# Performance work log

Measured on AMD Instinct MI355X. Metric: run time of the kernel, lower is better.

## Reference

```python
import jax, jax.numpy as jnp
import numpy as np

B, S, D = 4, 2048, 768
LN_EPS = 1e-12


def setup_inputs() -> dict:
    key = jax.random.key(0)
    k0, k1, k2, k3 = jax.random.split(key, 4)
    scale = 1.0 / np.sqrt(D).astype(np.float32)
    return {
        "hidden_states": jax.random.normal(k0, (B, S, D), jnp.float32),
        "attention_mask": jnp.ones((B, 1, S, S), jnp.int32),
        "prior_n_attn": jax.random.uniform(k1, (B, S, S), jnp.float32),
        "ln_w": jnp.ones((D,), jnp.float32),
        "ln_b": jnp.zeros((D,), jnp.float32),
        "wq": jax.random.normal(k2, (D, D), jnp.float32) * scale,
        "bq": jnp.zeros((D,), jnp.float32),
        "wk": jax.random.normal(k3, (D, D), jnp.float32) * scale,
        "bk": jnp.zeros((D,), jnp.float32),
    }


def reference(hidden_states, attention_mask, prior_n_attn, ln_w, ln_b, wq, bq, wk, bk):
    _, S_, D_ = hidden_states.shape
    # LayerNorm (biased variance, as torch.nn.LayerNorm)
    mu = hidden_states.mean(-1, keepdims=True)
    var = ((hidden_states - mu) ** 2).mean(-1, keepdims=True)
    h = (hidden_states - mu) / jnp.sqrt(var + LN_EPS) * ln_w + ln_b

    a = jnp.eye(S_, k=1, dtype=jnp.int32)      # superdiagonal
    bI = jnp.eye(S_, dtype=jnp.int32)          # diagonal
    c = jnp.eye(S_, k=-1, dtype=jnp.int32)     # subdiagonal
    tri = jnp.triu(jnp.ones((S_, S_), jnp.float32))

    # mask & (a + c): band of width 1 off the diagonal; then squeeze dim 1
    mask = (attention_mask.astype(jnp.int32) & (a + c))[:, 0]  # [B,S,S]

    q = h @ wq + bq
    k = h @ wk + bk
    scores = jnp.einsum("bsd,btd->bst", q, k) / D_
    scores = jnp.where(mask == 0, -jnp.inf, scores)
    n = jnp.nan_to_num(jax.nn.softmax(scores, axis=-1))
    n = jnp.sqrt(n * jnp.swapaxes(n, -2, -1) + 1e-9)
    n = prior_n_attn + (1.0 - prior_n_attn) * n

    # keep only the superdiagonal of log(n + 1e-9); zero elsewhere
    logm = jnp.log(n + 1e-9) * a.astype(n.dtype)
    # prefix-sum via triangular matmuls (same math as torch source)
    t = logm @ tri                                   # [B,S,S]
    g = jnp.exp(jnp.einsum("ij,bjk->bik", tri, t))   # [B,S,S]
    su = tri - bI.astype(tri.dtype)                  # strictly-upper indicator
    g = g * su                                       # masked_fill((tri-b)==0, 0)
    diag_part = jnp.where(bI == 0, 1e-9, n)          # n.masked_fill(b==0, 1e-9)
    g = g + jnp.swapaxes(g, -2, -1) + diag_part
    return (g, n)
```

## Files before the change

kernel.cpp:

```cpp
#include <hip/hip_runtime.h>
#include <hip/hip_bf16.h>
#include <math.h>
#include <stdint.h>

#define BB 4
#define SS 2048
#define DD 768
#define MM (BB*SS)

typedef __attribute__((ext_vector_type(4))) float  f32x4;
typedef __attribute__((ext_vector_type(8))) __bf16 bf16x8;
typedef __attribute__((ext_vector_type(4))) __bf16 bf16x4;

#define AS1 __attribute__((address_space(1)))
#define AS3 __attribute__((address_space(3)))

__global__ __launch_bounds__(256) void wcvt_kernel(const float* __restrict__ wq,
        const float* __restrict__ wk, __bf16* __restrict__ Wqb, __bf16* __restrict__ Wkb) {
    const int bid = blockIdx.x;
    const float* src; __bf16* dst; int off;
    if (bid < 576) { src = wq; dst = Wqb; off = bid; }
    else           { src = wk; dst = Wkb; off = bid - 576; }
    const size_t e = ((size_t)off * 256 + threadIdx.x) * 4;
    f32x4 v = *(const f32x4*)(src + e);
    bf16x4 o;
#pragma unroll
    for (int c = 0; c < 4; c++) o[c] = (__bf16)v[c];
    *(bf16x4*)(dst + e) = o;
}

__global__ __launch_bounds__(256) void uvcb_kernel(const float* __restrict__ wq,
        const float* __restrict__ wk, const float* __restrict__ bq,
        const float* __restrict__ bk, float* __restrict__ u, float* __restrict__ v,
        float* __restrict__ cb) {
    const int bid = blockIdx.x;
    const int lane = threadIdx.x & 63, wv = threadIdx.x >> 6;
    if (bid == 384) {
        if (wv != 0) return;
        float s = 0.f;
#pragma unroll
        for (int m = 0; m < 12; m++) s += bq[lane + 64 * m] * bk[lane + 64 * m];
#pragma unroll
        for (int o = 1; o < 64; o <<= 1) s += __shfl_xor(s, o);
        if (lane == 0) cb[0] = s;
        return;
    }
    const bool isU = bid < 192;
    const int row = (isU ? bid : bid - 192) * 4 + wv;
    const float* W = isU ? wq : wk;
    const float* bvec = isU ? bk : bq;
    const float* wr = W + (size_t)row * DD;
    float s = 0.f;
#pragma unroll
    for (int m = 0; m < 12; m++) s += wr[lane + 64 * m] * bvec[lane + 64 * m];
#pragma unroll
    for (int o = 1; o < 64; o <<= 1) s += __shfl_xor(s, o);
    if (lane == 0) (isU ? u : v)[row] = s;
}

__global__ __launch_bounds__(256) void ln_kernel(const float* __restrict__ x,
        const float* __restrict__ lw, const float* __restrict__ lb,
        const float* __restrict__ u, const float* __restrict__ v,
        __bf16* __restrict__ h, float* __restrict__ Aarr, float* __restrict__ Barr) {
    const int row = blockIdx.x * 4 + (threadIdx.x >> 6);
    const int lane = threadIdx.x & 63;
    const float* xr = x + (size_t)row * DD + lane * 12;
    f32x4 a0 = *(const f32x4*)(xr), a1 = *(const f32x4*)(xr + 4), a2 = *(const f32x4*)(xr + 8);
    float xs[12];
#pragma unroll
    for (int c = 0; c < 4; c++) { xs[c] = a0[c]; xs[4 + c] = a1[c]; xs[8 + c] = a2[c]; }
    float s = 0.f, ss = 0.f;
#pragma unroll
    for (int c = 0; c < 12; c++) { s += xs[c]; ss += xs[c] * xs[c]; }
#pragma unroll
    for (int o = 1; o < 64; o <<= 1) { s += __shfl_xor(s, o); ss += __shfl_xor(ss, o); }
    const float mu = s * (1.0f / DD);
    const float var = ss * (1.0f / DD) - mu * mu;
    const float rstd = 1.0f / sqrtf(var + 1e-12f);
    const float* wp = lw + lane * 12; const float* bp = lb + lane * 12;
    const float* up = u + lane * 12;  const float* vp = v + lane * 12;
    f32x4 w0 = *(const f32x4*)(wp), w1 = *(const f32x4*)(wp + 4), w2 = *(const f32x4*)(wp + 8);
    f32x4 b0 = *(const f32x4*)(bp), b1 = *(const f32x4*)(bp + 4), b2 = *(const f32x4*)(bp + 8);
    f32x4 u0 = *(const f32x4*)(up), u1 = *(const f32x4*)(up + 4), u2 = *(const f32x4*)(up + 8);
    f32x4 v0 = *(const f32x4*)(vp), v1 = *(const f32x4*)(vp + 4), v2 = *(const f32x4*)(vp + 8);
    float wv[12], bv[12], uv[12], vv[12];
#pragma unroll
    for (int c = 0; c < 4; c++) {
        wv[c] = w0[c]; wv[4 + c] = w1[c]; wv[8 + c] = w2[c];
        bv[c] = b0[c]; bv[4 + c] = b1[c]; bv[8 + c] = b2[c];
        uv[c] = u0[c]; uv[4 + c] = u1[c]; uv[8 + c] = u2[c];
        vv[c] = v0[c]; vv[4 + c] = v1[c]; vv[8 + c] = v2[c];
    }
    bf16x4 o0, o1, o2;
    float ap = 0.f, bpv = 0.f;
#pragma unroll
    for (int c = 0; c < 12; c++) {
        const float y = (xs[c] - mu) * rstd * wv[c] + bv[c];
        ap += y * uv[c]; bpv += y * vv[c];
        if (c < 4) o0[c] = (__bf16)y; else if (c < 8) o1[c - 4] = (__bf16)y; else o2[c - 8] = (__bf16)y;
    }
    __bf16* hr = h + (size_t)row * DD + lane * 12;
    *(bf16x4*)(hr) = o0; *(bf16x4*)(hr + 4) = o1; *(bf16x4*)(hr + 8) = o2;
#pragma unroll
    for (int o = 1; o < 64; o <<= 1) { ap += __shfl_xor(ap, o); bpv += __shfl_xor(bpv, o); }
    if (lane == 0) { Aarr[row] = ap; Barr[row] = bpv; }
}

__global__ __launch_bounds__(256) void gemm768_kernel(const __bf16* __restrict__ A,
        const __bf16* __restrict__ Bt, __bf16* __restrict__ C) {
    __shared__ __attribute__((aligned(16))) __bf16 As[128][32];
    __shared__ __attribute__((aligned(16))) __bf16 Bs[128][32];
    const int m0 = blockIdx.x * 128;
    const int n0 = blockIdx.y * 128;
    const int t = threadIdx.x;
    const int wave = t >> 6, lane = t & 63;
    const int wr = wave >> 1, wc = wave & 1;
    f32x4 acc[4][4] = {};

    char* asb = (char*)&As[0][0];
    char* bsb = (char*)&Bs[0][0];
    const int c0  = wave * 64 + lane;
    const int rA0 = c0 >> 2;
    const int cA0 = (c0 & 3) << 3;

    for (int k0 = 0; k0 < DD; k0 += 32) {
        const __bf16* ga0 = A  + (size_t)(m0 + rA0) * DD + k0 + cA0;
        const __bf16* ga1 = ga0 + (size_t)64 * DD;
        const __bf16* gb0 = Bt + (size_t)(n0 + rA0) * DD + k0 + cA0;
        const __bf16* gb1 = gb0 + (size_t)64 * DD;
        __builtin_amdgcn_global_load_lds((const AS1 void*)(ga0), (AS3 void*)(asb + wave * 1024),        16, 0, 0);
        __builtin_amdgcn_global_load_lds((const AS1 void*)(ga1), (AS3 void*)(asb + 4096 + wave * 1024), 16, 0, 0);
        __builtin_amdgcn_global_load_lds((const AS1 void*)(gb0), (AS3 void*)(bsb + wave * 1024),        16, 0, 0);
        __builtin_amdgcn_global_load_lds((const AS1 void*)(gb1), (AS3 void*)(bsb + 4096 + wave * 1024), 16, 0, 0);
        __syncthreads();
        const int r = lane & 15, ko = (lane >> 4) << 3;
        bf16x8 af[4], bvf[4];
#pragma unroll
        for (int i = 0; i < 4; i++) af[i]  = *(const bf16x8*)&As[wr * 64 + i * 16 + r][ko];
#pragma unroll
        for (int j = 0; j < 4; j++) bvf[j] = *(const bf16x8*)&Bs[wc * 64 + j * 16 + r][ko];
#pragma unroll
        for (int i = 0; i < 4; i++)
#pragma unroll
            for (int j = 0; j < 4; j++)
                acc[i][j] = __builtin_amdgcn_mfma_f32_16x16x32_bf16(af[i], bvf[j], acc[i][j], 0, 0, 0);
        __syncthreads();
    }
#pragma unroll
    for (int i = 0; i < 4; i++) {
        const int mm = m0 + wr * 64 + i * 16 + (lane >> 4) * 4;
#pragma unroll
        for (int j = 0; j < 4; j++) {
            const int nn = n0 + wc * 64 + j * 16 + (lane & 15);
#pragma unroll
            for (int rr = 0; rr < 4; rr++)
                C[(size_t)(mm + rr) * DD + nn] = (__bf16)acc[i][j][rr];
        }
    }
}

__global__ __launch_bounds__(256) void band_kernel(const __bf16* __restrict__ h,
        const __bf16* __restrict__ R, const int* __restrict__ att,
        const float* __restrict__ Aarr, const float* __restrict__ Barr,
        const float* __restrict__ cbp, float* __restrict__ pu, float* __restrict__ pd) {
    const int idx  = blockIdx.x * 4 + (threadIdx.x >> 6);
    const int lane = threadIdx.x & 63;
    const int b = idx >> 11;
    const int s = idx & 2047;
    const __bf16* hp = h + (size_t)idx * DD + lane * 12;
    bf16x4 h0 = *(const bf16x4*)(hp), h1 = *(const bf16x4*)(hp + 4), h2 = *(const bf16x4*)(hp + 8);
    float hv[12];
#pragma unroll
    for (int c = 0; c < 4; c++) { hv[c] = (float)h0[c]; hv[4 + c] = (float)h1[c]; hv[8 + c] = (float)h2[c]; }
    float du = 0.f, dn = 0.f;
    if (s < SS - 1) {
        const __bf16* rp = R + (size_t)(idx + 1) * DD + lane * 12;
        bf16x4 r0 = *(const bf16x4*)(rp), r1 = *(const bf16x4*)(rp + 4), r2 = *(const bf16x4*)(rp + 8);
#pragma unroll
        for (int c = 0; c < 4; c++) {
            du += hv[c] * (float)r0[c];
            du += hv[4 + c] * (float)r1[c];
            du += hv[8 + c] * (float)r2[c];
        }
    }
    if (s > 0) {
        const __bf16* rp = R + (size_t)(idx - 1) * DD + lane * 12;
        bf16x4 r0 = *(const bf16x4*)(rp), r1 = *(const bf16x4*)(rp + 4), r2 = *(const bf16x4*)(rp + 8);
#pragma unroll
        for (int c = 0; c < 4; c++) {
            dn += hv[c] * (float)r0[c];
            dn += hv[4 + c] * (float)r1[c];
            dn += hv[8 + c] * (float)r2[c];
        }
    }
#pragma unroll
    for (int o = 1; o < 64; o <<= 1) { du += __shfl_xor(du, o); dn += __shfl_xor(dn, o); }
    if (lane == 0) {
        const float cb = cbp[0];
        const float As = Aarr[idx];
        const float eu = (du + As + ((s < SS - 1) ? Barr[idx + 1] : 0.f) + cb) * (1.0f / DD);
        const float ed = (dn + As + ((s > 0)      ? Barr[idx - 1] : 0.f) + cb) * (1.0f / DD);
        const bool au = (s < SS - 1) && ((att[((size_t)b * SS + s) * SS + (s + 1)] & 1) != 0);
        const bool ad = (s > 0)      && ((att[((size_t)b * SS + s) * SS + (s - 1)] & 1) != 0);
        float puv = 0.f, pdv = 0.f;
        if (au || ad) {
            float mx = au ? eu : ed;
            if (au && ad) mx = fmaxf(eu, ed);
            const float zu = au ? expf(eu - mx) : 0.f;
            const float zd = ad ? expf(ed - mx) : 0.f;
            const float iz = 1.f / (zu + zd);
            puv = zu * iz; pdv = zd * iz;
        }
        pu[idx] = puv; pd[idx] = pdv;
    }
}

__global__ __launch_bounds__(256) void scan_kernel(const float* __restrict__ pu,
        const float* __restrict__ pd, const float* __restrict__ prior,
        float* __restrict__ nb, double* __restrict__ P) {
    const int b = blockIdx.x;
    const int t = threadIdx.x;
    double L[8];
    double mysum = 0.0;
#pragma unroll
    for (int e = 0; e < 8; e++) {
        const int s = t * 8 + e;
        double Lv = 0.0;
        float nbv = 0.f;
        if (s < SS - 1) {
            const float a = pu[b * SS + s];
            const float c = pd[b * SS + s + 1];
            nbv = sqrtf(a * c + 1e-9f);
            const float pr = prior[(size_t)b * SS * SS + (size_t)s * SS + s + 1];
            const float nsup = pr + (1.f - pr) * nbv;
            Lv = log((double)nsup + 1e-9);
        }
        nb[b * SS + s] = nbv;
        L[e] = Lv; mysum += Lv;
    }
    __shared__ double warr[256];
    warr[t] = mysum;
    __syncthreads();
    for (int o = 1; o < 256; o <<= 1) {
        double v = 0.0;
        if (t >= o) v = warr[t - o];
        __syncthreads();
        if (t >= o) warr[t] += v;
        __syncthreads();
    }
    double run = warr[t] - mysum;
#pragma unroll
    for (int e = 0; e < 8; e++) {
        P[(size_t)b * SS + t * 8 + e] = run;
        run += L[e];
    }
}

__global__ __launch_bounds__(256) void out_kernel(const float* __restrict__ prior,
        const float* __restrict__ nb, const double* __restrict__ P,
        float* __restrict__ gout, float* __restrict__ nout) {
    const size_t f = (size_t)blockIdx.x * 256 + threadIdx.x;
    const int b = (int)(f >> 20);
    const size_t r = f & 1048575;
    const int i  = (int)(r >> 9);
    const int k4 = (int)(r & 511) * 4;
    const f32x4 pv = *(const f32x4*)(prior + (f << 2));
    const double Pi = P[(size_t)b * SS + i];
    f32x4 nres, gres;
#pragma unroll
    for (int c = 0; c < 4; c++) {
        const int k = k4 + c;
        const float pr = pv[c];
        float v = 3.16227766016838e-5f;
        if (k == i + 1)      v = nb[b * SS + i];
        else if (k == i - 1) v = nb[b * SS + k];
        const float nval = pr + (1.f - pr) * v;
        nres[c] = nval;
        float g;
        if (k == i) {
            g = nval;
        } else {
            const double Pk = P[(size_t)b * SS + k];
            const double dd = (k > i) ? (Pk - Pi) : (Pi - Pk);
            g = expf((float)dd) + 1e-9f;
        }
        gres[c] = g;
    }
    *(f32x4*)(gout + (f << 2)) = gres;
    *(f32x4*)(nout + (f << 2)) = nres;
}

extern "C" void kernel_launch(void* const* d_in, const int* in_sizes, int n_in,
                              void* d_out, int out_size, void* d_ws, size_t ws_size,
                              hipStream_t stream) {
    const float* hs    = (const float*)d_in[0];
    const int*   att   = (const int*)d_in[1];
    const float* prior = (const float*)d_in[2];
    const float* ln_w  = (const float*)d_in[3];
    const float* ln_b  = (const float*)d_in[4];
    const float* wq    = (const float*)d_in[5];
    const float* bq    = (const float*)d_in[6];
    const float* wk    = (const float*)d_in[7];
    const float* bk    = (const float*)d_in[8];

    float* gout = (float*)d_out;
    float* nout = gout + (size_t)BB * SS * SS;

    char* ws = (char*)d_ws;
    __bf16* h    = (__bf16*)(ws);
    __bf16* Wqb  = (__bf16*)(ws + 12582912);
    __bf16* Wkb  = (__bf16*)(ws + 13762560);
    __bf16* G    = (__bf16*)(ws + 14942208);
    __bf16* R    = (__bf16*)(ws + 16121856);
    float*  u    = (float*) (ws + 28704768);
    float*  v    = (float*) (ws + 28707840);
    float*  Aarr = (float*) (ws + 28710912);
    float*  Barr = (float*) (ws + 28743680);
    float*  cb   = (float*) (ws + 28776448);
    float*  pu   = (float*) (ws + 28776704);
    float*  pd   = (float*) (ws + 28809472);
    float*  nbuf = (float*) (ws + 28842240);
    double* P    = (double*)(ws + 28875008);

    wcvt_kernel<<<dim3(1152), dim3(256), 0, stream>>>(wq, wk, Wqb, Wkb);
    uvcb_kernel<<<dim3(385), dim3(256), 0, stream>>>(wq, wk, bq, bk, u, v, cb);
    ln_kernel<<<dim3(MM / 4), dim3(256), 0, stream>>>(hs, ln_w, ln_b, u, v, h, Aarr, Barr);
    gemm768_kernel<<<dim3(6, 6), dim3(256), 0, stream>>>(Wqb, Wkb, G);
    gemm768_kernel<<<dim3(MM / 128, 6), dim3(256), 0, stream>>>(h, G, R);
    band_kernel<<<dim3(MM / 4), dim3(256), 0, stream>>>(h, R, att, Aarr, Barr, cb, pu, pd);
    scan_kernel<<<dim3(BB), dim3(256), 0, stream>>>(pu, pd, prior, nbuf, P);
    out_kernel<<<dim3((BB * SS * SS / 4) / 256), dim3(256), 0, stream>>>(prior, nbuf, P, gout, nout);
}
```

Before: 110.8 us.

## Fuse weight prep into one kernel, fold biases into epilogues, widen output kernel

```diff
diff --git a/kernel.cpp b/kernel.cpp
--- a/kernel.cpp
+++ b/kernel.cpp
@@ -15,53 +15,97 @@
 #define AS1 __attribute__((address_space(1)))
 #define AS3 __attribute__((address_space(3)))
 
-__global__ __launch_bounds__(256) void wcvt_kernel(const float* __restrict__ wq,
-        const float* __restrict__ wk, __bf16* __restrict__ Wqb, __bf16* __restrict__ Wkb) {
+__global__ __launch_bounds__(256) void prep_kernel(const float* __restrict__ wq,
+        const float* __restrict__ wk, const float* __restrict__ bq,
+        const float* __restrict__ bk, __bf16* __restrict__ G,
+        float* __restrict__ u, float* __restrict__ v, float* __restrict__ cb) {
+    __shared__ __attribute__((aligned(16))) __bf16 As[128][32];
+    __shared__ __attribute__((aligned(16))) __bf16 Bs[128][32];
     const int bid = blockIdx.x;
-    const float* src; __bf16* dst; int off;
-    if (bid < 576) { src = wq; dst = Wqb; off = bid; }
-    else           { src = wk; dst = Wkb; off = bid - 576; }
-    const size_t e = ((size_t)off * 256 + threadIdx.x) * 4;
-    f32x4 v = *(const f32x4*)(src + e);
-    bf16x4 o;
-#pragma unroll
-    for (int c = 0; c < 4; c++) o[c] = (__bf16)v[c];
-    *(bf16x4*)(dst + e) = o;
-}
-
-__global__ __launch_bounds__(256) void uvcb_kernel(const float* __restrict__ wq,
-        const float* __restrict__ wk, const float* __restrict__ bq,
-        const float* __restrict__ bk, float* __restrict__ u, float* __restrict__ v,
-        float* __restrict__ cb) {
-    const int bid = blockIdx.x;
-    const int lane = threadIdx.x & 63, wv = threadIdx.x >> 6;
-    if (bid == 384) {
-        if (wv != 0) return;
+    if (bid >= 36) {
+        const int id = bid - 36;
+        const int lane = threadIdx.x & 63, wv_ = threadIdx.x >> 6;
+        if (id == 384) {
+            if (wv_ != 0) return;
+            float s = 0.f;
+#pragma unroll
+            for (int m = 0; m < 12; m++) s += bq[lane + 64 * m] * bk[lane + 64 * m];
+#pragma unroll
+            for (int o = 1; o < 64; o <<= 1) s += __shfl_xor(s, o);
+            if (lane == 0) cb[0] = s;
+            return;
+        }
+        const bool isU = id < 192;
+        const int row = (isU ? id : id - 192) * 4 + wv_;
+        const float* W = isU ? wq : wk;
+        const float* bvec = isU ? bk : bq;
+        const float* wr_ = W + (size_t)row * DD;
         float s = 0.f;
 #pragma unroll
-        for (int m = 0; m < 12; m++) s += bq[lane + 64 * m] * bk[lane + 64 * m];
+        for (int m = 0; m < 12; m++) s += wr_[lane + 64 * m] * bvec[lane + 64 * m];
 #pragma unroll
         for (int o = 1; o < 64; o <<= 1) s += __shfl_xor(s, o);
-        if (lane == 0) cb[0] = s;
+        if (lane == 0) (isU ? u : v)[row] = s;
         return;
     }
-    const bool isU = bid < 192;
-    const int row = (isU ? bid : bid - 192) * 4 + wv;
-    const float* W = isU ? wq : wk;
-    const float* bvec = isU ? bk : bq;
-    const float* wr = W + (size_t)row * DD;
-    float s = 0.f;
-#pragma unroll
-    for (int m = 0; m < 12; m++) s += wr[lane + 64 * m] * bvec[lane + 64 * m];
-#pragma unroll
-    for (int o = 1; o < 64; o <<= 1) s += __shfl_xor(s, o);
-    if (lane == 0) (isU ? u : v)[row] = s;
+    const int m0 = (bid % 6) * 128;
+    const int n0 = (bid / 6) * 128;
+    const int t = threadIdx.x;
+    const int wave = t >> 6, lane = t & 63;
+    const int wr = wave >> 1, wc = wave & 1;
+    const int srow = t >> 1, shalf = (t & 1) * 16;
+    f32x4 acc[4][4] = {};
+
+    for (int k0 = 0; k0 < DD; k0 += 32) {
+        const float* ga = wq + (size_t)(m0 + srow) * DD + k0 + shalf;
+        const float* gb = wk + (size_t)(n0 + srow) * DD + k0 + shalf;
+        f32x4 a0 = *(const f32x4*)(ga),     a1 = *(const f32x4*)(ga + 4);
+        f32x4 a2 = *(const f32x4*)(ga + 8), a3 = *(const f32x4*)(ga + 12);
+        f32x4 b0 = *(const f32x4*)(gb),     b1 = *(const f32x4*)(gb + 4);
+        f32x4 b2 = *(const f32x4*)(gb + 8), b3 = *(const f32x4*)(gb + 12);
+        bf16x8 av0, av1, bv0, bv1;
+#pragma unroll
+        for (int c = 0; c < 4; c++) {
+            av0[c] = (__bf16)a0[c]; av0[4 + c] = (__bf16)a1[c];
+            av1[c] = (__bf16)a2[c]; av1[4 + c] = (__bf16)a3[c];
+            bv0[c] = (__bf16)b0[c]; bv0[4 + c] = (__bf16)b1[c];
+            bv1[c] = (__bf16)b2[c]; bv1[4 + c] = (__bf16)b3[c];
+        }
+        __syncthreads();
+        *(bf16x8*)&As[srow][shalf]     = av0;
+        *(bf16x8*)&As[srow][shalf + 8] = av1;
+        *(bf16x8*)&Bs[srow][shalf]     = bv0;
+        *(bf16x8*)&Bs[srow][shalf + 8] = bv1;
+        __syncthreads();
+        const int r = lane & 15, ko = (lane >> 4) << 3;
+        bf16x8 af[4], bvf[4];
+#pragma unroll
+        for (int i = 0; i < 4; i++) af[i]  = *(const bf16x8*)&As[wr * 64 + i * 16 + r][ko];
+#pragma unroll
+        for (int j = 0; j < 4; j++) bvf[j] = *(const bf16x8*)&Bs[wc * 64 + j * 16 + r][ko];
+#pragma unroll
+        for (int i = 0; i < 4; i++)
+#pragma unroll
+            for (int j = 0; j < 4; j++)
+                acc[i][j] = __builtin_amdgcn_mfma_f32_16x16x32_bf16(af[i], bvf[j], acc[i][j], 0, 0, 0);
+    }
+#pragma unroll
+    for (int i = 0; i < 4; i++) {
+        const int mm = m0 + wr * 64 + i * 16 + (lane >> 4) * 4;
+#pragma unroll
+        for (int j = 0; j < 4; j++) {
+            const int nn = n0 + wc * 64 + j * 16 + (lane & 15);
+#pragma unroll
+            for (int rr = 0; rr < 4; rr++)
+                G[(size_t)(mm + rr) * DD + nn] = (__bf16)acc[i][j][rr];
+        }
+    }
 }
 
 __global__ __launch_bounds__(256) void ln_kernel(const float* __restrict__ x,
         const float* __restrict__ lw, const float* __restrict__ lb,
-        const float* __restrict__ u, const float* __restrict__ v,
-        __bf16* __restrict__ h, float* __restrict__ Aarr, float* __restrict__ Barr) {
+        const float* __restrict__ v, const float* __restrict__ cbp,
+        __bf16* __restrict__ h, float* __restrict__ Barr) {
     const int row = blockIdx.x * 4 + (threadIdx.x >> 6);
     const int lane = threadIdx.x & 63;
     const float* xr = x + (size_t)row * DD + lane * 12;
@@ -78,36 +122,35 @@
     const float var = ss * (1.0f / DD) - mu * mu;
     const float rstd = 1.0f / sqrtf(var + 1e-12f);
     const float* wp = lw + lane * 12; const float* bp = lb + lane * 12;
-    const float* up = u + lane * 12;  const float* vp = v + lane * 12;
+    const float* vp = v + lane * 12;
     f32x4 w0 = *(const f32x4*)(wp), w1 = *(const f32x4*)(wp + 4), w2 = *(const f32x4*)(wp + 8);
     f32x4 b0 = *(const f32x4*)(bp), b1 = *(const f32x4*)(bp + 4), b2 = *(const f32x4*)(bp + 8);
-    f32x4 u0 = *(const f32x4*)(up), u1 = *(const f32x4*)(up + 4), u2 = *(const f32x4*)(up + 8);
     f32x4 v0 = *(const f32x4*)(vp), v1 = *(const f32x4*)(vp + 4), v2 = *(const f32x4*)(vp + 8);
-    float wv[12], bv[12], uv[12], vv[12];
+    float wv[12], bv[12], vv[12];
 #pragma unroll
     for (int c = 0; c < 4; c++) {
         wv[c] = w0[c]; wv[4 + c] = w1[c]; wv[8 + c] = w2[c];
         bv[c] = b0[c]; bv[4 + c] = b1[c]; bv[8 + c] = b2[c];
-        uv[c] = u0[c]; uv[4 + c] = u1[c]; uv[8 + c] = u2[c];
         vv[c] = v0[c]; vv[4 + c] = v1[c]; vv[8 + c] = v2[c];
     }
     bf16x4 o0, o1, o2;
-    float ap = 0.f, bpv = 0.f;
+    float bpv = 0.f;
 #pragma unroll
     for (int c = 0; c < 12; c++) {
         const float y = (xs[c] - mu) * rstd * wv[c] + bv[c];
-        ap += y * uv[c]; bpv += y * vv[c];
+        bpv += y * vv[c];
         if (c < 4) o0[c] = (__bf16)y; else if (c < 8) o1[c - 4] = (__bf16)y; else o2[c - 8] = (__bf16)y;
     }
     __bf16* hr = h + (size_t)row * DD + lane * 12;
     *(bf16x4*)(hr) = o0; *(bf16x4*)(hr + 4) = o1; *(bf16x4*)(hr + 8) = o2;
 #pragma unroll
-    for (int o = 1; o < 64; o <<= 1) { ap += __shfl_xor(ap, o); bpv += __shfl_xor(bpv, o); }
-    if (lane == 0) { Aarr[row] = ap; Barr[row] = bpv; }
-}
-
-__global__ __launch_bounds__(256) void gemm768_kernel(const __bf16* __restrict__ A,
-        const __bf16* __restrict__ Bt, __bf16* __restrict__ C) {
+    for (int o = 1; o < 64; o <<= 1) bpv += __shfl_xor(bpv, o);
+    if (lane == 0) Barr[row] = bpv + cbp[0];
+}
+
+__global__ __launch_bounds__(256) void rgemm_kernel(const __bf16* __restrict__ A,
+        const __bf16* __restrict__ Bt, const float* __restrict__ u,
+        __bf16* __restrict__ C) {
     __shared__ __attribute__((aligned(16))) __bf16 As[128][32];
     __shared__ __attribute__((aligned(16))) __bf16 Bs[128][32];
     const int m0 = blockIdx.x * 128;
@@ -152,21 +195,24 @@
 #pragma unroll
         for (int j = 0; j < 4; j++) {
             const int nn = n0 + wc * 64 + j * 16 + (lane & 15);
+            const float bias = u[nn];
 #pragma unroll
             for (int rr = 0; rr < 4; rr++)
-                C[(size_t)(mm + rr) * DD + nn] = (__bf16)acc[i][j][rr];
+                C[(size_t)(mm + rr) * DD + nn] = (__bf16)(acc[i][j][rr] + bias);
         }
     }
 }
 
 __global__ __launch_bounds__(256) void band_kernel(const __bf16* __restrict__ h,
         const __bf16* __restrict__ R, const int* __restrict__ att,
-        const float* __restrict__ Aarr, const float* __restrict__ Barr,
-        const float* __restrict__ cbp, float* __restrict__ pu, float* __restrict__ pd) {
+        const float* __restrict__ Barr, const float* __restrict__ prior,
+        float* __restrict__ pu, float* __restrict__ pd, float* __restrict__ prsup) {
     const int idx  = blockIdx.x * 4 + (threadIdx.x >> 6);
     const int lane = threadIdx.x & 63;
     const int b = idx >> 11;
     const int s = idx & 2047;
+    if (lane == 1 && s < SS - 1)
+        prsup[idx] = prior[((size_t)b * SS + s) * SS + s + 1];
     const __bf16* hp = h + (size_t)idx * DD + lane * 12;
     bf16x4 h0 = *(const bf16x4*)(hp), h1 = *(const bf16x4*)(hp + 4), h2 = *(const bf16x4*)(hp + 8);
     float hv[12];
@@ -196,10 +242,8 @@
 #pragma unroll
     for (int o = 1; o < 64; o <<= 1) { du += __shfl_xor(du, o); dn += __shfl_xor(dn, o); }
     if (lane == 0) {
-        const float cb = cbp[0];
-        const float As = Aarr[idx];
-        const float eu = (du + As + ((s < SS - 1) ? Barr[idx + 1] : 0.f) + cb) * (1.0f / DD);
-        const float ed = (dn + As + ((s > 0)      ? Barr[idx - 1] : 0.f) + cb) * (1.0f / DD);
+        const float eu = (du + ((s < SS - 1) ? Barr[idx + 1] : 0.f)) * (1.0f / DD);
+        const float ed = (dn + ((s > 0)      ? Barr[idx - 1] : 0.f)) * (1.0f / DD);
         const bool au = (s < SS - 1) && ((att[((size_t)b * SS + s) * SS + (s + 1)] & 1) != 0);
         const bool ad = (s > 0)      && ((att[((size_t)b * SS + s) * SS + (s - 1)] & 1) != 0);
         float puv = 0.f, pdv = 0.f;
@@ -216,8 +260,8 @@
 }
 
 __global__ __launch_bounds__(256) void scan_kernel(const float* __restrict__ pu,
-        const float* __restrict__ pd, const float* __restrict__ prior,
-        float* __restrict__ nb, double* __restrict__ P) {
+        const float* __restrict__ pd, const float* __restrict__ prsup,
+        float* __restrict__ nb, double* __restrict__ P2) {
     const int b = blockIdx.x;
     const int t = threadIdx.x;
     double L[8];
@@ -231,9 +275,9 @@
             const float a = pu[b * SS + s];
             const float c = pd[b * SS + s + 1];
             nbv = sqrtf(a * c + 1e-9f);
-            const float pr = prior[(size_t)b * SS * SS + (size_t)s * SS + s + 1];
+            const float pr = prsup[b * SS + s];
             const float nsup = pr + (1.f - pr) * nbv;
-            Lv = log((double)nsup + 1e-9);
+            Lv = (double)log2f(nsup + 1e-9f);
         }
         nb[b * SS + s] = nbv;
         L[e] = Lv; mysum += Lv;
@@ -251,43 +295,49 @@
     double run = warr[t] - mysum;
 #pragma unroll
     for (int e = 0; e < 8; e++) {
-        P[(size_t)b * SS + t * 8 + e] = run;
+        P2[(size_t)b * SS + t * 8 + e] = run;
         run += L[e];
     }
 }
 
 __global__ __launch_bounds__(256) void out_kernel(const float* __restrict__ prior,
-        const float* __restrict__ nb, const double* __restrict__ P,
+        const float* __restrict__ nb, const double* __restrict__ P2,
         float* __restrict__ gout, float* __restrict__ nout) {
-    const size_t f = (size_t)blockIdx.x * 256 + threadIdx.x;
-    const int b = (int)(f >> 20);
-    const size_t r = f & 1048575;
-    const int i  = (int)(r >> 9);
-    const int k4 = (int)(r & 511) * 4;
-    const f32x4 pv = *(const f32x4*)(prior + (f << 2));
-    const double Pi = P[(size_t)b * SS + i];
-    f32x4 nres, gres;
-#pragma unroll
-    for (int c = 0; c < 4; c++) {
-        const int k = k4 + c;
-        const float pr = pv[c];
-        float v = 3.16227766016838e-5f;
-        if (k == i + 1)      v = nb[b * SS + i];
-        else if (k == i - 1) v = nb[b * SS + k];
-        const float nval = pr + (1.f - pr) * v;
-        nres[c] = nval;
+    const size_t t8 = (size_t)blockIdx.x * 256 + threadIdx.x;
+    const int b = (int)(t8 >> 19);
+    const size_t off = t8 << 3;
+    const size_t r = off & ((1u << 22) - 1);
+    const int i  = (int)(r >> 11);
+    const int k0 = (int)(r & 2047);
+    const f32x4 p0 = *(const f32x4*)(prior + off);
+    const f32x4 p1 = *(const f32x4*)(prior + off + 4);
+    const double* Pb = P2 + ((size_t)b << 11);
+    const double Pi = Pb[i];
+    const float* nbb = nb + ((size_t)b << 11);
+    f32x4 g0, g1, n0, n1;
+#pragma unroll
+    for (int c = 0; c < 8; c++) {
+        const int k = k0 + c;
+        const float pr = (c < 4) ? p0[c] : p1[c - 4];
+        float vv = 3.16227766016838e-5f;
+        if (k == i + 1)      vv = nbb[i];
+        else if (k == i - 1) vv = nbb[k];
+        const float nval = pr + (1.f - pr) * vv;
         float g;
         if (k == i) {
             g = nval;
         } else {
-            const double Pk = P[(size_t)b * SS + k];
+            const double Pk = Pb[k];
             const double dd = (k > i) ? (Pk - Pi) : (Pi - Pk);
-            g = expf((float)dd) + 1e-9f;
-        }
-        gres[c] = g;
-    }
-    *(f32x4*)(gout + (f << 2)) = gres;
-    *(f32x4*)(nout + (f << 2)) = nres;
+            g = exp2f((float)dd) + 1e-9f;
+        }
+        if (c < 4) { g0[c] = g; n0[c] = nval; }
+        else       { g1[c - 4] = g; n1[c - 4] = nval; }
+    }
+    *(f32x4*)(gout + off)     = g0;
+    *(f32x4*)(gout + off + 4) = g1;
+    *(f32x4*)(nout + off)     = n0;
+    *(f32x4*)(nout + off + 4) = n1;
 }
 
 extern "C" void kernel_launch(void* const* d_in, const int* in_sizes, int n_in,
@@ -307,27 +357,23 @@
     float* nout = gout + (size_t)BB * SS * SS;
 
     char* ws = (char*)d_ws;
-    __bf16* h    = (__bf16*)(ws);
-    __bf16* Wqb  = (__bf16*)(ws + 12582912);
-    __bf16* Wkb  = (__bf16*)(ws + 13762560);
-    __bf16* G    = (__bf16*)(ws + 14942208);
-    __bf16* R    = (__bf16*)(ws + 16121856);
-    float*  u    = (float*) (ws + 28704768);
-    float*  v    = (float*) (ws + 28707840);
-    float*  Aarr = (float*) (ws + 28710912);
-    float*  Barr = (float*) (ws + 28743680);
-    float*  cb   = (float*) (ws + 28776448);
-    float*  pu   = (float*) (ws + 28776704);
-    float*  pd   = (float*) (ws + 28809472);
-    float*  nbuf = (float*) (ws + 28842240);
-    double* P    = (double*)(ws + 28875008);
-
-    wcvt_kernel<<<dim3(1152), dim3(256), 0, stream>>>(wq, wk, Wqb, Wkb);
-    uvcb_kernel<<<dim3(385), dim3(256), 0, stream>>>(wq, wk, bq, bk, u, v, cb);
-    ln_kernel<<<dim3(MM / 4), dim3(256), 0, stream>>>(hs, ln_w, ln_b, u, v, h, Aarr, Barr);
-    gemm768_kernel<<<dim3(6, 6), dim3(256), 0, stream>>>(Wqb, Wkb, G);
-    gemm768_kernel<<<dim3(MM / 128, 6), dim3(256), 0, stream>>>(h, G, R);
-    band_kernel<<<dim3(MM / 4), dim3(256), 0, stream>>>(h, R, att, Aarr, Barr, cb, pu, pd);
-    scan_kernel<<<dim3(BB), dim3(256), 0, stream>>>(pu, pd, prior, nbuf, P);
-    out_kernel<<<dim3((BB * SS * SS / 4) / 256), dim3(256), 0, stream>>>(prior, nbuf, P, gout, nout);
-}
+    __bf16* h     = (__bf16*)(ws);
+    __bf16* G     = (__bf16*)(ws + 12582912);
+    __bf16* R     = (__bf16*)(ws + 13762560);
+    float*  u     = (float*) (ws + 26345472);
+    float*  v     = (float*) (ws + 26348544);
+    float*  cbp   = (float*) (ws + 26351616);
+    float*  Barr  = (float*) (ws + 26351872);
+    float*  pu    = (float*) (ws + 26384640);
+    float*  pd    = (float*) (ws + 26417408);
+    float*  nbuf  = (float*) (ws + 26450176);
+    float*  prsup = (float*) (ws + 26482944);
+    double* P2    = (double*)(ws + 26515712);
+
+    prep_kernel<<<dim3(421), dim3(256), 0, stream>>>(wq, wk, bq, bk, G, u, v, cbp);
+    ln_kernel<<<dim3(MM / 4), dim3(256), 0, stream>>>(hs, ln_w, ln_b, v, cbp, h, Barr);
+    rgemm_kernel<<<dim3(MM / 128, 6), dim3(256), 0, stream>>>(h, G, u, R);
+    band_kernel<<<dim3(MM / 4), dim3(256), 0, stream>>>(h, R, att, Barr, prior, pu, pd, prsup);
+    scan_kernel<<<dim3(BB), dim3(256), 0, stream>>>(pu, pd, prsup, nbuf, P2);
+    out_kernel<<<dim3((BB * SS * SS / 8) / 256), dim3(256), 0, stream>>>(prior, nbuf, P2, gout, nout);
+}
```

New measurement: 120.4 us. +8.7%, slower.
